# Kernel optimization log

Hardware: AMD Instinct MI355X
Metric: run time of the kernel (lower is better)

## Reference

```python
import jax, jax.numpy as jnp
import numpy as np

B, S, H = 2, 256, 768
LR = 0.01
EPS = 1e-5  # torch LayerNorm default


def setup_inputs() -> dict:
    key = jax.random.key(0)
    ks = jax.random.split(key, 6)
    f = jnp.float32
    return {
        "x": jax.random.normal(ks[0], (B, S, H), f),
        "W_init": jax.random.normal(ks[1], (H, H), f) * 0.02,
        "b_init": jnp.zeros((H,), f),
        "gate_w": jax.random.normal(ks[2], (4 * H, H), f) * 0.02,
        "gate_b": jnp.zeros((4 * H,), f),
        "up_w": jax.random.normal(ks[3], (4 * H, H), f) * 0.02,
        "up_b": jnp.zeros((4 * H,), f),
        "down_w": jax.random.normal(ks[4], (H, 4 * H), f) * 0.02,
        "down_b": jnp.zeros((H,), f),
        "norm_w": jnp.ones((H,), f),
        "norm_b": jnp.zeros((H,), f),
    }


def _layernorm(x, w, b):
    mu = jnp.mean(x, axis=-1, keepdims=True)
    var = jnp.var(x, axis=-1, keepdims=True)
    return (x - mu) * jax.lax.rsqrt(var + EPS) * w + b


def reference(x, W_init, b_init, gate_w, gate_b, up_w, up_b,
              down_w, down_b, norm_w, norm_b):
    # x: [B, S, H]. Sequential TTT fast-weight recurrence, vectorized over batch,
    # scanned over time (equivalent to the per-token Python loop in torch).
    Bn, Sn, Hn = x.shape
    xs = jnp.swapaxes(x, 0, 1)                                   # [S, B, H]
    x_next = jnp.concatenate([xs[1:], jnp.zeros_like(xs[:1])], 0)  # target x[t+1]
    # lr per step; the update is skipped at the last token (t == S-1)
    lr = jnp.concatenate([jnp.full((Sn - 1,), LR, x.dtype),
                          jnp.zeros((1,), x.dtype)])

    W0 = jnp.broadcast_to(W_init, (Bn, Hn, Hn))
    b0 = jnp.broadcast_to(b_init, (Bn, Hn))

    def step(carry, inp):
        W, b = carry
        xt, xn, lr_t = inp
        pred = jnp.einsum('bij,bj->bi', W, xt) + b               # fast-weight matvec
        gated = jax.nn.sigmoid(pred @ gate_w.T + gate_b) * (pred @ up_w.T + up_b)
        out = _layernorm(gated @ down_w.T + down_b + pred, norm_w, norm_b)
        diff = pred - xn                                         # prediction error
        W = W - lr_t * diff[:, :, None] * xt[:, None, :]         # rank-1 update
        b = b - lr_t * diff
        return (W, b), out

    _, ys = jax.lax.scan(step, (W0, b0), (xs, x_next, lr))       # ys: [S, B, H]
    return jnp.swapaxes(ys, 0, 1)
```

## Files before the change

kernel.cpp:

```cpp
#include <hip/hip_runtime.h>
#include <hip/hip_bf16.h>

#define H   768
#define H4  3072
#define S   256
#define BB  2
#define M   (BB * S)
#define LRC 0.01f
#define C   64
#define NC  (S / C)

typedef __attribute__((ext_vector_type(8))) short bf16x8;
typedef __attribute__((ext_vector_type(4))) float f32x4;

__device__ inline short bfbits(float f) {
    __hip_bfloat16 h = __float2bfloat16(f);
    return *reinterpret_cast<short*>(&h);
}

__global__ __launch_bounds__(256) void k_stage(
    const float* __restrict__ x,  const float* __restrict__ W0,
    const float* __restrict__ gw, const float* __restrict__ uw,
    const float* __restrict__ dw,
    short* __restrict__ Xhi, short* __restrict__ Xlo,
    short* __restrict__ Whi, short* __restrict__ Wlo,
    short* __restrict__ gw2, short* __restrict__ uw2, short* __restrict__ dw2)
{
    const long gid = (long)blockIdx.x * 256 + threadIdx.x;
    const float* src; short* hp; short* lp = nullptr; long base;
    if (gid < 98304)        { src = x;  hp = Xhi; lp = Xlo; base = 0; }
    else if (gid < 245760)  { src = W0; hp = Whi; lp = Wlo; base = 98304; }
    else if (gid < 835584)  { src = gw; hp = gw2; base = 245760; }
    else if (gid < 1425408) { src = uw; hp = uw2; base = 835584; }
    else                    { src = dw; hp = dw2; base = 1425408; }
    const long i = (gid - base) * 4;
    const float4 v = *(const float4*)(src + i);
    const float vf[4] = {v.x, v.y, v.z, v.w};
    short h4[4], l4[4];
#pragma unroll
    for (int j = 0; j < 4; ++j) {
        h4[j] = bfbits(vf[j]);
        __hip_bfloat16 hb = *reinterpret_cast<__hip_bfloat16*>(&h4[j]);
        l4[j] = bfbits(vf[j] - __bfloat162float(hb));
    }
    *(uint2*)(hp + i) = *(uint2*)h4;
    if (lp) *(uint2*)(lp + i) = *(uint2*)l4;
}

__global__ __launch_bounds__(256) void k_gram_base(
    const short* __restrict__ Xhi, const short* __restrict__ Xlo,
    const short* __restrict__ Whi, const short* __restrict__ Wlo,
    const float* __restrict__ b0,
    float* __restrict__ g, float* __restrict__ base0)
{
    const int wid = threadIdx.x >> 6, lane = threadIdx.x & 63;
    const int r16 = lane & 15, quad = lane >> 4;
    const int id = blockIdx.x;

    f32x4 acc[4];
#pragma unroll
    for (int i = 0; i < 4; ++i) acc[i] = (f32x4){0, 0, 0, 0};

    if (id < 32) {
        const int bx = id & 3, by = (id >> 2) & 3, b = id >> 4;
        const int m0 = by * 64, n0 = bx * 64 + wid * 16;
        const short* XH = Xhi + b * S * H;
        const short* XL = Xlo + b * S * H;
        for (int k0 = 0; k0 < H; k0 += 32) {
            const int k = k0 + quad * 8;
            const bf16x8 bh = *(const bf16x8*)(XH + (n0 + r16) * H + k);
            const bf16x8 bl = *(const bf16x8*)(XL + (n0 + r16) * H + k);
#pragma unroll
            for (int i = 0; i < 4; ++i) {
                const bf16x8 ah = *(const bf16x8*)(XH + (m0 + i * 16 + r16) * H + k);
                const bf16x8 al = *(const bf16x8*)(XL + (m0 + i * 16 + r16) * H + k);
                acc[i] = __builtin_amdgcn_mfma_f32_16x16x32_bf16(ah, bh, acc[i], 0, 0, 0);
                acc[i] = __builtin_amdgcn_mfma_f32_16x16x32_bf16(ah, bl, acc[i], 0, 0, 0);
                acc[i] = __builtin_amdgcn_mfma_f32_16x16x32_bf16(al, bh, acc[i], 0, 0, 0);
            }
        }
        const int col = n0 + r16;
#pragma unroll
        for (int i = 0; i < 4; ++i)
#pragma unroll
            for (int r = 0; r < 4; ++r) {
                const int row = m0 + i * 16 + quad * 4 + r;
                g[(b * S + row) * S + col] = acc[i][r] + 1.f;
            }
    } else {
        const int id2 = id - 32;
        const int m0 = (id2 / 12) * 64, n0 = (id2 % 12) * 64 + wid * 16;
        for (int k0 = 0; k0 < H; k0 += 32) {
            const int k = k0 + quad * 8;
            const bf16x8 bh = *(const bf16x8*)(Whi + (n0 + r16) * H + k);
            const bf16x8 bl = *(const bf16x8*)(Wlo + (n0 + r16) * H + k);
#pragma unroll
            for (int i = 0; i < 4; ++i) {
                const bf16x8 ah = *(const bf16x8*)(Xhi + (m0 + i * 16 + r16) * H + k);
                const bf16x8 al = *(const bf16x8*)(Xlo + (m0 + i * 16 + r16) * H + k);
                acc[i] = __builtin_amdgcn_mfma_f32_16x16x32_bf16(ah, bh, acc[i], 0, 0, 0);
                acc[i] = __builtin_amdgcn_mfma_f32_16x16x32_bf16(ah, bl, acc[i], 0, 0, 0);
                acc[i] = __builtin_amdgcn_mfma_f32_16x16x32_bf16(al, bh, acc[i], 0, 0, 0);
            }
        }
        const int col = n0 + r16;
        const float bv = b0[col];
#pragma unroll
        for (int i = 0; i < 4; ++i)
#pragma unroll
            for (int r = 0; r < 4; ++r) {
                const int row = m0 + i * 16 + quad * 4 + r;
                base0[row * H + col] = acc[i][r] + bv;
            }
    }
}

__global__ __launch_bounds__(256) void k_recur3(
    const float* __restrict__ x,
    const float* __restrict__ base0,
    const float* __restrict__ g,
    float* __restrict__ pred_f,
    __hip_bfloat16* __restrict__ pred_h)
{
    __shared__ float tB[64 * 17];
    __shared__ float tX[64 * 17];
    __shared__ float Dl[256 * 17];
    __shared__ float Gs[64 * 65];
    const int tid = threadIdx.x;
    const int w = tid >> 6, lane = tid & 63;
    const int b = blockIdx.x / 48, hb = blockIdx.x % 48;
    const int h0 = hb * 16;
    const int ho = w * 4;
    const int ct = tid >> 2;
    const int cq = (tid & 3) * 4;

    for (int c = 0; c < NC; ++c) {
        const int t0 = c * C;
        __syncthreads();
        {
            const int gm = b * S + t0 + ct;
            const float4 bv = *(const float4*)(base0 + gm * H + h0 + cq);
            float4 xv = {0.f, 0.f, 0.f, 0.f};
            if (t0 + ct + 1 < S)
                xv = *(const float4*)(x + (gm + 1) * H + h0 + cq);
            tB[ct * 17 + cq + 0] = bv.x - xv.x;
            tB[ct * 17 + cq + 1] = bv.y - xv.y;
            tB[ct * 17 + cq + 2] = bv.z - xv.z;
            tB[ct * 17 + cq + 3] = bv.w - xv.w;
            tX[ct * 17 + cq + 0] = xv.x;
            tX[ct * 17 + cq + 1] = xv.y;
            tX[ct * 17 + cq + 2] = xv.z;
            tX[ct * 17 + cq + 3] = xv.w;
#pragma unroll
            for (int j = 0; j < 16; ++j) {
                const int idx = tid + 256 * j;
                const int row = idx >> 6, col = idx & 63;
                Gs[row * 65 + col] = g[(long)(b * S + t0 + row) * S + t0 + col];
            }
        }
        __syncthreads();
        float R[4], Xn[4];
#pragma unroll
        for (int h = 0; h < 4; ++h) {
            R[h]  = tB[lane * 17 + ho + h];
            Xn[h] = tX[lane * 17 + ho + h];
        }
        const float* gcol = g + (long)(b * S) * S + t0 + lane;
#pragma unroll 4
        for (int cs = 0; cs < t0; ++cs) {
            const float Gv = gcol[(long)cs * S];
            const float* dr = &Dl[cs * 17 + ho];
            R[0] -= LRC * Gv * dr[0];
            R[1] -= LRC * Gv * dr[1];
            R[2] -= LRC * Gv * dr[2];
            R[3] -= LRC * Gv * dr[3];
        }
        for (int s = 0; s < C; ++s) {
            float dsb[4];
#pragma unroll
            for (int h = 0; h < 4; ++h) dsb[h] = __shfl(R[h], s, 64);
            const float Gv = Gs[s * 65 + lane];
            const float mlt = (lane > s) ? LRC : 0.f;
#pragma unroll
            for (int h = 0; h < 4; ++h) R[h] -= mlt * Gv * dsb[h];
        }
#pragma unroll
        for (int h = 0; h < 4; ++h) Dl[(t0 + lane) * 17 + ho + h] = R[h];
        __syncthreads();
#pragma unroll
        for (int h = 0; h < 4; ++h) tB[lane * 17 + ho + h] = R[h] + Xn[h];
        __syncthreads();
        {
            const int gm = b * S + t0 + ct;
            float4 pv;
            pv.x = tB[ct * 17 + cq + 0];
            pv.y = tB[ct * 17 + cq + 1];
            pv.z = tB[ct * 17 + cq + 2];
            pv.w = tB[ct * 17 + cq + 3];
            *(float4*)(pred_f + gm * H + h0 + cq) = pv;
            short p4[4];
            p4[0] = bfbits(pv.x); p4[1] = bfbits(pv.y);
            p4[2] = bfbits(pv.z); p4[3] = bfbits(pv.w);
            *(uint2*)((short*)pred_h + gm * H + h0 + cq) = *(uint2*)p4;
        }
    }
}

#define RS 40
__global__ __launch_bounds__(256) void k_gateup3(
    const __hip_bfloat16* __restrict__ predh,
    const short* __restrict__ gwp, const float* __restrict__ gb,
    const short* __restrict__ uwp, const float* __restrict__ ub,
    __hip_bfloat16* __restrict__ hid)
{
    __shared__ int4 smv[1600];
    short* sm = (short*)smv;
    short* sA = sm;
    short* sG = sm + 64 * RS;
    short* sU = sm + (64 + 128) * RS;

    const int tid = threadIdx.x;
    const int wid = tid >> 6, lane = tid & 63;
    const int r16 = lane & 15, quad = lane >> 4;
    const int wm = wid & 1, wn = wid >> 1;
    const int n0 = blockIdx.x * 128;
    const int m0 = blockIdx.y * 64;

    const int srow = tid >> 2;
    const int sch  = (tid & 3) * 8;
    const short* A = (const short*)predh;

    f32x4 ag[2][4], au[2][4];
#pragma unroll
    for (int i = 0; i < 2; ++i)
#pragma unroll
        for (int j = 0; j < 4; ++j) { ag[i][j] = (f32x4){0,0,0,0}; au[i][j] = (f32x4){0,0,0,0}; }

    int4 rA, rG0, rG1, rU0, rU1;
    {
        const int k = sch;
        rA  = *(const int4*)(A   + (m0 + srow) * H + k);
        rG0 = *(const int4*)(gwp + (n0 + srow) * H + k);
        rG1 = *(const int4*)(gwp + (n0 + 64 + srow) * H + k);
        rU0 = *(const int4*)(uwp + (n0 + srow) * H + k);
        rU1 = *(const int4*)(uwp + (n0 + 64 + srow) * H + k);
    }
    for (int it = 0; it < 24; ++it) {
        *(int4*)(sA + srow * RS + sch)        = rA;
        *(int4*)(sG + srow * RS + sch)        = rG0;
        *(int4*)(sG + (64 + srow) * RS + sch) = rG1;
        *(int4*)(sU + srow * RS + sch)        = rU0;
        *(int4*)(sU + (64 + srow) * RS + sch) = rU1;
        __syncthreads();
        if (it < 23) {
            const int k = (it + 1) * 32 + sch;
            rA  = *(const int4*)(A   + (m0 + srow) * H + k);
            rG0 = *(const int4*)(gwp + (n0 + srow) * H + k);
            rG1 = *(const int4*)(gwp + (n0 + 64 + srow) * H + k);
            rU0 = *(const int4*)(uwp + (n0 + srow) * H + k);
            rU1 = *(const int4*)(uwp + (n0 + 64 + srow) * H + k);
        }
        bf16x8 aF[2], gF[4], uF[4];
#pragma unroll
        for (int i = 0; i < 2; ++i)
            aF[i] = *(const bf16x8*)(sA + (wm * 32 + i * 16 + r16) * RS + quad * 8);
#pragma unroll
        for (int j = 0; j < 4; ++j) {
            gF[j] = *(const bf16x8*)(sG + (wn * 64 + j * 16 + r16) * RS + quad * 8);
            uF[j] = *(const bf16x8*)(sU + (wn * 64 + j * 16 + r16) * RS + quad * 8);
        }
#pragma unroll
        for (int i = 0; i < 2; ++i)
#pragma unroll
            for (int j = 0; j < 4; ++j) {
                ag[i][j] = __builtin_amdgcn_mfma_f32_16x16x32_bf16(aF[i], gF[j], ag[i][j], 0, 0, 0);
                au[i][j] = __builtin_amdgcn_mfma_f32_16x16x32_bf16(aF[i], uF[j], au[i][j], 0, 0, 0);
            }
        __syncthreads();
    }
#pragma unroll
    for (int j = 0; j < 4; ++j) {
        const int ocol = n0 + wn * 64 + j * 16 + r16;
        const float gbv = gb[ocol], ubv = ub[ocol];
#pragma unroll
        for (int i = 0; i < 2; ++i)
#pragma unroll
            for (int r = 0; r < 4; ++r) {
                const int orow = m0 + wm * 32 + i * 16 + quad * 4 + r;
                const float gg = ag[i][j][r] + gbv;
                const float u  = au[i][j][r] + ubv;
                const float sg = 1.f / (1.f + __expf(-gg));
                hid[orow * H4 + ocol] = __float2bfloat16(sg * u);
            }
    }
}

__device__ inline bf16x8 ldb32(const void* p, long off) {
    const float* f = (const float*)p + off;
    const float4 a = *(const float4*)f;
    const float4 b = *(const float4*)(f + 4);
    bf16x8 r;
    r[0] = bfbits(a.x); r[1] = bfbits(a.y); r[2] = bfbits(a.z); r[3] = bfbits(a.w);
    r[4] = bfbits(b.x); r[5] = bfbits(b.y); r[6] = bfbits(b.z); r[7] = bfbits(b.w);
    return r;
}
__device__ inline bf16x8 ldb16(const void* p, long off) {
    return *(const bf16x8*)((const short*)p + off);
}

template<bool WB>
__global__ __launch_bounds__(256) void k_gateup2(
    const __hip_bfloat16* __restrict__ predh,
    const void* __restrict__ gw, const float* __restrict__ gb,
    const void* __restrict__ uw, const float* __restrict__ ub,
    __hip_bfloat16* __restrict__ hid)
{
    const int wid = threadIdx.x >> 6, lane = threadIdx.x & 63;
    const int r16 = lane & 15, quad = lane >> 4;
    const int m0 = blockIdx.y * 64;
    const int n0 = blockIdx.x * 64 + wid * 16;

    f32x4 ag[4], au[4];
#pragma unroll
    for (int i = 0; i < 4; ++i) { ag[i] = (f32x4){0,0,0,0}; au[i] = (f32x4){0,0,0,0}; }
    const short* A = (const short*)predh;
    const long brow = (long)(n0 + r16) * H;

    for (int k0 = 0; k0 < H; k0 += 32) {
        const int k = k0 + quad * 8;
        const bf16x8 bg = WB ? ldb16(gw, brow + k) : ldb32(gw, brow + k);
        const bf16x8 bu = WB ? ldb16(uw, brow + k) : ldb32(uw, brow + k);
#pragma unroll
        for (int i = 0; i < 4; ++i) {
            const bf16x8 af = *(const bf16x8*)(A + (m0 + i * 16 + r16) * H + k);
            ag[i] = __builtin_amdgcn_mfma_f32_16x16x32_bf16(af, bg, ag[i], 0, 0, 0);
            au[i] = __builtin_amdgcn_mfma_f32_16x16x32_bf16(af, bu, au[i], 0, 0, 0);
        }
    }
    const int ocol = n0 + r16;
    const float gbv = gb[ocol], ubv = ub[ocol];
#pragma unroll
    for (int i = 0; i < 4; ++i)
#pragma unroll
        for (int r = 0; r < 4; ++r) {
            const int orow = m0 + i * 16 + quad * 4 + r;
            const float gg = ag[i][r] + gbv;
            const float u = au[i][r] + ubv;
            const float sg = 1.f / (1.f + __expf(-gg));
            hid[orow * H4 + ocol] = __float2bfloat16(sg * u);
        }
}

template<bool WB>
__global__ __launch_bounds__(256) void k_down2(
    const __hip_bfloat16* __restrict__ hid,
    const void* __restrict__ dw, const float* __restrict__ db,
    const float* __restrict__ predf, float* __restrict__ dout)
{
    const int wid = threadIdx.x >> 6, lane = threadIdx.x & 63;
    const int r16 = lane & 15, quad = lane >> 4;
    const int m0 = blockIdx.y * 32;
    const int n0 = blockIdx.x * 64 + wid * 16;

    f32x4 ac[2];
    ac[0] = (f32x4){0,0,0,0}; ac[1] = (f32x4){0,0,0,0};
    const short* A = (const short*)hid;
    const long brow = (long)(n0 + r16) * H4;

    for (int k0 = 0; k0 < H4; k0 += 32) {
        const int k = k0 + quad * 8;
        const bf16x8 bd = WB ? ldb16(dw, brow + k) : ldb32(dw, brow + k);
#pragma unroll
        for (int i = 0; i < 2; ++i) {
            const bf16x8 af = *(const bf16x8*)(A + (m0 + i * 16 + r16) * H4 + k);
            ac[i] = __builtin_amdgcn_mfma_f32_16x16x32_bf16(af, bd, ac[i], 0, 0, 0);
        }
    }
    const int ocol = n0 + r16;
    const float dbv = db[ocol];
#pragma unroll
    for (int i = 0; i < 2; ++i)
#pragma unroll
        for (int r = 0; r < 4; ++r) {
            const int orow = m0 + i * 16 + quad * 4 + r;
            dout[orow * H + ocol] = ac[i][r] + dbv + predf[orow * H + ocol];
        }
}

__global__ __launch_bounds__(256) void k_ln(
    const float* __restrict__ dout,
    const float* __restrict__ nw,
    const float* __restrict__ nb,
    float* __restrict__ out)
{
    const int m = blockIdx.x;
    const int tid = threadIdx.x;
    const float* rowp = dout + m * H;

    float v[3];
    float s = 0.f, s2 = 0.f;
#pragma unroll
    for (int j = 0; j < 3; ++j) {
        v[j] = rowp[tid + 256 * j];
        s += v[j];
        s2 += v[j] * v[j];
    }
#pragma unroll
    for (int off = 32; off >= 1; off >>= 1) {
        s  += __shfl_xor(s, off, 64);
        s2 += __shfl_xor(s2, off, 64);
    }
    __shared__ float rs[4], rs2[4];
    const int wid = tid >> 6, lane = tid & 63;
    if (lane == 0) { rs[wid] = s; rs2[wid] = s2; }
    __syncthreads();
    s  = rs[0] + rs[1] + rs[2] + rs[3];
    s2 = rs2[0] + rs2[1] + rs2[2] + rs2[3];
    const float mu  = s / (float)H;
    const float var = s2 / (float)H - mu * mu;
    const float inv = rsqrtf(var + 1e-5f);
#pragma unroll
    for (int j = 0; j < 3; ++j) {
        const int hh = tid + 256 * j;
        out[m * H + hh] = (v[j] - mu) * inv * nw[hh] + nb[hh];
    }
}

extern "C" void kernel_launch(void* const* d_in, const int* in_sizes, int n_in,
                              void* d_out, int out_size, void* d_ws, size_t ws_size,
                              hipStream_t stream)
{
    const float* x   = (const float*)d_in[0];
    const float* W0  = (const float*)d_in[1];
    const float* b0  = (const float*)d_in[2];
    const float* gw  = (const float*)d_in[3];
    const float* gb  = (const float*)d_in[4];
    const float* uw  = (const float*)d_in[5];
    const float* ub  = (const float*)d_in[6];
    const float* dw  = (const float*)d_in[7];
    const float* db  = (const float*)d_in[8];
    const float* nw  = (const float*)d_in[9];
    const float* nb  = (const float*)d_in[10];

    char* ws = (char*)d_ws;
    float*          pred_f = (float*)(ws);
    __hip_bfloat16* pred_h = (__hip_bfloat16*)(ws + 1572864);
    __hip_bfloat16* hid    = (__hip_bfloat16*)(ws + 2359296);
    float*          base0  = (float*)(ws + 5505024);
    float*          dout_f = (float*)(ws + 5505024);
    float*          g      = (float*)(ws + 7077888);
    short*          Xhi    = (short*)(ws + 7602176);
    short*          Xlo    = (short*)(ws + 8388608);
    short*          Whi    = (short*)(ws + 9175040);
    short*          Wlo    = (short*)(ws + 10354688);
    const size_t WNEED = 11534336ULL + 3ULL * 4718592ULL;
    const bool wb = ws_size >= WNEED;
    short* gw2 = (short*)(ws + 11534336);
    short* uw2 = (short*)(ws + 11534336 + 4718592);
    short* dw2 = (short*)(ws + 11534336 + 2 * 4718592);

    const int ngroups = wb ? 2015232 : 245760;
    k_stage<<<dim3(ngroups / 256), 256, 0, stream>>>(
        x, W0, gw, uw, dw, Xhi, Xlo, Whi, Wlo, gw2, uw2, dw2);
    k_gram_base<<<dim3(128), 256, 0, stream>>>(Xhi, Xlo, Whi, Wlo, b0, g, base0);
    k_recur3<<<dim3(96), 256, 0, stream>>>(x, base0, g, pred_f, pred_h);
    if (wb) {
        k_gateup3<<<dim3(H4 / 128, M / 64), 256, 0, stream>>>(pred_h, gw2, gb, uw2, ub, hid);
        k_down2<true><<<dim3(H / 64, M / 32), 256, 0, stream>>>(hid, dw2, db, pred_f, dout_f);
    } else {
        k_gateup2<false><<<dim3(H4 / 64, M / 64), 256, 0, stream>>>(pred_h, gw, gb, uw, ub, hid);
        k_down2<false><<<dim3(H / 64, M / 32), 256, 0, stream>>>(hid, dw, db, pred_f, dout_f);
    }
    k_ln<<<dim3(M), 256, 0, stream>>>(dout_f, nw, nb, (float*)d_out);
}
```

Baseline: 227.3 us.

## Precompute per-chunk triangular inverse and use LDS-tiled down projection

```diff
diff --git a/kernel.cpp b/kernel.cpp
--- a/kernel.cpp
+++ b/kernel.cpp
@@ -115,17 +115,55 @@
     }
 }
 
-__global__ __launch_bounds__(256) void k_recur3(
+__global__ __launch_bounds__(256) void k_inv(
+    const float* __restrict__ g, float* __restrict__ U)
+{
+    __shared__ float Gi[C * 65];
+    const int tid = threadIdx.x;
+    const int w = tid >> 6, lane = tid & 63;
+    const int b = blockIdx.x >> 2, c = blockIdx.x & 3;
+    const int t0 = c * C;
+
+#pragma unroll
+    for (int j = 0; j < 16; ++j) {
+        const int idx = tid + 256 * j;
+        const int row = idx >> 6, col = idx & 63;
+        Gi[row * 65 + col] = g[(long)(b * S + t0 + row) * S + t0 + col];
+    }
+    __syncthreads();
+
+    const int j0 = w * 16;
+    float R[16];
+#pragma unroll
+    for (int i = 0; i < 16; ++i) R[i] = (lane == j0 + i) ? 1.f : 0.f;
+
+    for (int s = 0; s < C - 1; ++s) {
+        const float Gv = Gi[s * 65 + lane];
+        const float mlt = (lane > s) ? LRC : 0.f;
+#pragma unroll
+        for (int i = 0; i < 16; ++i) {
+            const float dsb = __shfl(R[i], s, 64);
+            R[i] -= mlt * Gv * dsb;
+        }
+    }
+    float* Ub = U + (long)(b * NC + c) * C * C;
+#pragma unroll
+    for (int i = 0; i < 16; ++i)
+        Ub[lane * C + j0 + i] = R[i];
+}
+
+__global__ __launch_bounds__(256) void k_recur4(
     const float* __restrict__ x,
     const float* __restrict__ base0,
     const float* __restrict__ g,
+    const float* __restrict__ U,
     float* __restrict__ pred_f,
     __hip_bfloat16* __restrict__ pred_h)
 {
     __shared__ float tB[64 * 17];
     __shared__ float tX[64 * 17];
     __shared__ float Dl[256 * 17];
-    __shared__ float Gs[64 * 65];
+    __shared__ float Us[64 * 65];
     const int tid = threadIdx.x;
     const int w = tid >> 6, lane = tid & 63;
     const int b = blockIdx.x / 48, hb = blockIdx.x % 48;
@@ -151,11 +189,12 @@
             tX[ct * 17 + cq + 1] = xv.y;
             tX[ct * 17 + cq + 2] = xv.z;
             tX[ct * 17 + cq + 3] = xv.w;
+            const float* Ub = U + (long)(b * NC + c) * C * C;
 #pragma unroll
             for (int j = 0; j < 16; ++j) {
                 const int idx = tid + 256 * j;
                 const int row = idx >> 6, col = idx & 63;
-                Gs[row * 65 + col] = g[(long)(b * S + t0 + row) * S + t0 + col];
+                Us[row * 65 + col] = Ub[row * C + col];
             }
         }
         __syncthreads();
@@ -175,20 +214,21 @@
             R[2] -= LRC * Gv * dr[2];
             R[3] -= LRC * Gv * dr[3];
         }
+        float D[4] = {0.f, 0.f, 0.f, 0.f};
+#pragma unroll 8
         for (int s = 0; s < C; ++s) {
-            float dsb[4];
-#pragma unroll
-            for (int h = 0; h < 4; ++h) dsb[h] = __shfl(R[h], s, 64);
-            const float Gv = Gs[s * 65 + lane];
-            const float mlt = (lane > s) ? LRC : 0.f;
-#pragma unroll
-            for (int h = 0; h < 4; ++h) R[h] -= mlt * Gv * dsb[h];
-        }
-#pragma unroll
-        for (int h = 0; h < 4; ++h) Dl[(t0 + lane) * 17 + ho + h] = R[h];
-        __syncthreads();
-#pragma unroll
-        for (int h = 0; h < 4; ++h) tB[lane * 17 + ho + h] = R[h] + Xn[h];
+            const float Gv = Us[lane * 65 + s];
+#pragma unroll
+            for (int h = 0; h < 4; ++h) {
+                const float dsb = __shfl(R[h], s, 64);
+                D[h] += Gv * dsb;
+            }
+        }
+#pragma unroll
+        for (int h = 0; h < 4; ++h) Dl[(t0 + lane) * 17 + ho + h] = D[h];
+        __syncthreads();
+#pragma unroll
+        for (int h = 0; h < 4; ++h) tB[lane * 17 + ho + h] = D[h] + Xn[h];
         __syncthreads();
         {
             const int gm = b * S + t0 + ct;
@@ -295,6 +335,72 @@
     }
 }
 
+__global__ __launch_bounds__(256) void k_down3(
+    const __hip_bfloat16* __restrict__ hid,
+    const short* __restrict__ dwp, const float* __restrict__ db,
+    const float* __restrict__ predf, float* __restrict__ dout)
+{
+    __shared__ int4 smv[640];
+    short* sm = (short*)smv;
+    short* sA = sm;
+    short* sB = sm + 64 * RS;
+
+    const int tid = threadIdx.x;
+    const int wid = tid >> 6, lane = tid & 63;
+    const int r16 = lane & 15, quad = lane >> 4;
+    const int wm = wid & 1, wn = wid >> 1;
+    const int n0 = blockIdx.x * 64;
+    const int m0 = blockIdx.y * 64;
+
+    const int srow = tid >> 2;
+    const int sch  = (tid & 3) * 8;
+    const short* A = (const short*)hid;
+
+    f32x4 ac[2][2];
+#pragma unroll
+    for (int i = 0; i < 2; ++i)
+#pragma unroll
+        for (int j = 0; j < 2; ++j) ac[i][j] = (f32x4){0,0,0,0};
+
+    int4 rA, rB;
+    rA = *(const int4*)(A   + (m0 + srow) * H4 + sch);
+    rB = *(const int4*)(dwp + (n0 + srow) * H4 + sch);
+    for (int it = 0; it < 96; ++it) {
+        *(int4*)(sA + srow * RS + sch) = rA;
+        *(int4*)(sB + srow * RS + sch) = rB;
+        __syncthreads();
+        if (it < 95) {
+            const int k = (it + 1) * 32 + sch;
+            rA = *(const int4*)(A   + (m0 + srow) * H4 + k);
+            rB = *(const int4*)(dwp + (n0 + srow) * H4 + k);
+        }
+        bf16x8 aF[2], bF[2];
+#pragma unroll
+        for (int i = 0; i < 2; ++i) {
+            aF[i] = *(const bf16x8*)(sA + (wm * 32 + i * 16 + r16) * RS + quad * 8);
+            bF[i] = *(const bf16x8*)(sB + (wn * 32 + i * 16 + r16) * RS + quad * 8);
+        }
+#pragma unroll
+        for (int i = 0; i < 2; ++i)
+#pragma unroll
+            for (int j = 0; j < 2; ++j)
+                ac[i][j] = __builtin_amdgcn_mfma_f32_16x16x32_bf16(aF[i], bF[j], ac[i][j], 0, 0, 0);
+        __syncthreads();
+    }
+#pragma unroll
+    for (int j = 0; j < 2; ++j) {
+        const int ocol = n0 + wn * 32 + j * 16 + r16;
+        const float dbv = db[ocol];
+#pragma unroll
+        for (int i = 0; i < 2; ++i)
+#pragma unroll
+            for (int r = 0; r < 4; ++r) {
+                const int orow = m0 + wm * 32 + i * 16 + quad * 4 + r;
+                dout[orow * H + ocol] = ac[i][j][r] + dbv + predf[orow * H + ocol];
+            }
+    }
+}
+
 __device__ inline bf16x8 ldb32(const void* p, long off) {
     const float* f = (const float*)p + off;
     const float4 a = *(const float4*)f;
@@ -304,11 +410,7 @@
     r[4] = bfbits(b.x); r[5] = bfbits(b.y); r[6] = bfbits(b.z); r[7] = bfbits(b.w);
     return r;
 }
-__device__ inline bf16x8 ldb16(const void* p, long off) {
-    return *(const bf16x8*)((const short*)p + off);
-}
-
-template<bool WB>
+
 __global__ __launch_bounds__(256) void k_gateup2(
     const __hip_bfloat16* __restrict__ predh,
     const void* __restrict__ gw, const float* __restrict__ gb,
@@ -328,8 +430,8 @@
 
     for (int k0 = 0; k0 < H; k0 += 32) {
         const int k = k0 + quad * 8;
-        const bf16x8 bg = WB ? ldb16(gw, brow + k) : ldb32(gw, brow + k);
-        const bf16x8 bu = WB ? ldb16(uw, brow + k) : ldb32(uw, brow + k);
+        const bf16x8 bg = ldb32(gw, brow + k);
+        const bf16x8 bu = ldb32(uw, brow + k);
 #pragma unroll
         for (int i = 0; i < 4; ++i) {
             const bf16x8 af = *(const bf16x8*)(A + (m0 + i * 16 + r16) * H + k);
@@ -351,8 +453,7 @@
         }
 }
 
-template<bool WB>
-__global__ __launch_bounds__(256) void k_down2(
+__global__ __launch_bounds__(256) void k_down2f(
     const __hip_bfloat16* __restrict__ hid,
     const void* __restrict__ dw, const float* __restrict__ db,
     const float* __restrict__ predf, float* __restrict__ dout)
@@ -369,7 +470,7 @@
 
     for (int k0 = 0; k0 < H4; k0 += 32) {
         const int k = k0 + quad * 8;
-        const bf16x8 bd = WB ? ldb16(dw, brow + k) : ldb32(dw, brow + k);
+        const bf16x8 bd = ldb32(dw, brow + k);
 #pragma unroll
         for (int i = 0; i < 2; ++i) {
             const bf16x8 af = *(const bf16x8*)(A + (m0 + i * 16 + r16) * H4 + k);
@@ -453,23 +554,25 @@
     short*          Xlo    = (short*)(ws + 8388608);
     short*          Whi    = (short*)(ws + 9175040);
     short*          Wlo    = (short*)(ws + 10354688);
-    const size_t WNEED = 11534336ULL + 3ULL * 4718592ULL;
+    float*          U      = (float*)(ws + 11534336);
+    const size_t WNEED = 11665408ULL + 3ULL * 4718592ULL;
     const bool wb = ws_size >= WNEED;
-    short* gw2 = (short*)(ws + 11534336);
-    short* uw2 = (short*)(ws + 11534336 + 4718592);
-    short* dw2 = (short*)(ws + 11534336 + 2 * 4718592);
+    short* gw2 = (short*)(ws + 11665408);
+    short* uw2 = (short*)(ws + 11665408 + 4718592);
+    short* dw2 = (short*)(ws + 11665408 + 2 * 4718592);
 
     const int ngroups = wb ? 2015232 : 245760;
     k_stage<<<dim3(ngroups / 256), 256, 0, stream>>>(
         x, W0, gw, uw, dw, Xhi, Xlo, Whi, Wlo, gw2, uw2, dw2);
     k_gram_base<<<dim3(128), 256, 0, stream>>>(Xhi, Xlo, Whi, Wlo, b0, g, base0);
-    k_recur3<<<dim3(96), 256, 0, stream>>>(x, base0, g, pred_f, pred_h);
+    k_inv<<<dim3(BB * NC), 256, 0, stream>>>(g, U);
+    k_recur4<<<dim3(96), 256, 0, stream>>>(x, base0, g, U, pred_f, pred_h);
     if (wb) {
         k_gateup3<<<dim3(H4 / 128, M / 64), 256, 0, stream>>>(pred_h, gw2, gb, uw2, ub, hid);
-        k_down2<true><<<dim3(H / 64, M / 32), 256, 0, stream>>>(hid, dw2, db, pred_f, dout_f);
+        k_down3<<<dim3(H / 64, M / 64), 256, 0, stream>>>(hid, dw2, db, pred_f, dout_f);
     } else {
-        k_gateup2<false><<<dim3(H4 / 64, M / 64), 256, 0, stream>>>(pred_h, gw, gb, uw, ub, hid);
-        k_down2<false><<<dim3(H / 64, M / 32), 256, 0, stream>>>(hid, dw, db, pred_f, dout_f);
+        k_gateup2<<<dim3(H4 / 64, M / 64), 256, 0, stream>>>(pred_h, gw, gb, uw, ub, hid);
+        k_down2f<<<dim3(H / 64, M / 32), 256, 0, stream>>>(hid, dw, db, pred_f, dout_f);
     }
     k_ln<<<dim3(M), 256, 0, stream>>>(dout_f, nw, nb, (float*)d_out);
 }
```

Result: slower. 238.3 us (+4.8%).
